# Kernel optimization log

Hardware: AMD Instinct MI355X
Metric: run time of the kernel (lower is better)

The kernel has to match this reference:

```python
import jax, jax.numpy as jnp
import numpy as np

N = 50000        # nodes
E = 800000       # edges (before self loops)
G = 512          # graphs
H = 2            # heads
FIN = 128        # in_features
CH = 64          # hidden per head
COUT = 32        # out_features
NEG_SLOPE = 0.2  # PyG GATConv default
BN_EPS = 1e-5


def _gat(x, src, dst, W, a_src, a_dst, b, concat, n):
    # x: [n, F], W: [F, H*C], a_src/a_dst: [H, C]
    h = (x @ W).reshape(n, a_src.shape[0], a_src.shape[1])        # [n, H, C]
    e = jax.nn.leaky_relu((h * a_src).sum(-1)[src]
                          + (h * a_dst).sum(-1)[dst], NEG_SLOPE)  # [Etot, H]
    # per-destination segment softmax (self loops guarantee nonempty segments)
    m = jax.ops.segment_max(e, dst, num_segments=n)
    ex = jnp.exp(e - m[dst])
    s = jax.ops.segment_sum(ex, dst, num_segments=n)
    alpha = ex / (s[dst] + 1e-16)                                 # [Etot, H]
    out = jax.ops.segment_sum(h[src] * alpha[:, :, None], dst, num_segments=n)
    out = out.reshape(n, -1) if concat else out.mean(axis=1)
    return out + b


def _bn(x, gamma, beta, mean, var):
    # BatchNorm1d in eval mode (running statistics)
    return (x - mean) * jax.lax.rsqrt(var + BN_EPS) * gamma + beta


def setup_inputs() -> dict:
    key = jax.random.key(0)
    ks = jax.random.split(key, 12)
    x = jax.random.normal(ks[0], (N, FIN), dtype=jnp.float32)
    edge_index = jax.random.randint(ks[1], (2, E), 0, N, dtype=jnp.int32)
    batch = jnp.sort(jax.random.randint(ks[2], (N,), 0, G, dtype=jnp.int32))
    inp = {"x": x, "edge_index": edge_index, "batch": batch}
    # layer 1: GATConv(FIN -> CH, heads=H, concat=True)
    inp["W1"] = jax.random.normal(ks[3], (FIN, H * CH), dtype=jnp.float32) * 0.1
    inp["as1"] = jax.random.normal(ks[4], (H, CH), dtype=jnp.float32) * 0.1
    inp["ad1"] = jax.random.normal(ks[5], (H, CH), dtype=jnp.float32) * 0.1
    inp["b1"] = jnp.zeros((H * CH,), dtype=jnp.float32)
    inp["bn1_gamma"] = jnp.ones((H * CH,), dtype=jnp.float32)
    inp["bn1_beta"] = jnp.zeros((H * CH,), dtype=jnp.float32)
    inp["bn1_mean"] = jax.random.normal(ks[6], (H * CH,), dtype=jnp.float32) * 0.05
    inp["bn1_var"] = jnp.ones((H * CH,), dtype=jnp.float32)
    # layer 2: GATConv(H*CH -> COUT, heads=H, concat=False)
    inp["W2"] = jax.random.normal(ks[7], (H * CH, H * COUT), dtype=jnp.float32) * 0.1
    inp["as2"] = jax.random.normal(ks[8], (H, COUT), dtype=jnp.float32) * 0.1
    inp["ad2"] = jax.random.normal(ks[9], (H, COUT), dtype=jnp.float32) * 0.1
    inp["b2"] = jnp.zeros((COUT,), dtype=jnp.float32)
    inp["bn2_gamma"] = jnp.ones((COUT,), dtype=jnp.float32)
    inp["bn2_beta"] = jnp.zeros((COUT,), dtype=jnp.float32)
    inp["bn2_mean"] = jax.random.normal(ks[10], (COUT,), dtype=jnp.float32) * 0.05
    inp["bn2_var"] = jnp.ones((COUT,), dtype=jnp.float32)
    return inp


def reference(x, edge_index, batch,
              W1, as1, ad1, b1, bn1_gamma, bn1_beta, bn1_mean, bn1_var,
              W2, as2, ad2, b2, bn2_gamma, bn2_beta, bn2_mean, bn2_var):
    n = x.shape[0]
    sl = jnp.arange(n, dtype=edge_index.dtype)
    src = jnp.concatenate([edge_index[0], sl])  # PyG add_self_loops=True
    dst = jnp.concatenate([edge_index[1], sl])
    h = _gat(x, src, dst, W1, as1, ad1, b1, True, n)
    h = jax.nn.relu(_bn(h, bn1_gamma, bn1_beta, bn1_mean, bn1_var))
    h = _gat(h, src, dst, W2, as2, ad2, b2, False, n)
    h = _bn(h, bn2_gamma, bn2_beta, bn2_mean, bn2_var)
    # global mean pool over graphs
    sums = jax.ops.segment_sum(h, batch, num_segments=G)
    cnts = jax.ops.segment_sum(jnp.ones((n,), h.dtype), batch, num_segments=G)
    pooled = sums / jnp.maximum(cnts, 1.0)[:, None]
    return jax.nn.log_softmax(pooled, axis=1)
```

## Files before the change

### kernel.cpp

```cpp
#include <hip/hip_runtime.h>
#include <hip/hip_bf16.h>

#define NEG_SLOPE 0.2f
#define BN_EPS 1e-5f
#define BSHIFT 7
#define P_PART 256
#define MAXB 512

typedef unsigned int uint32;
typedef unsigned short ushort16;
typedef __attribute__((ext_vector_type(8))) short bf16x8;
typedef __attribute__((ext_vector_type(4))) float f32x4;
typedef __attribute__((ext_vector_type(2))) float f32x2;

__device__ __forceinline__ ushort16 f2bf(float f) {
    uint32 u = __float_as_uint(f);
    u = (u + 0x7fff + ((u >> 16) & 1)) >> 16;
    return (ushort16)u;
}

__device__ __forceinline__ f32x2 pkfma(f32x2 ex2, uint32 u, f32x2 acc) {
    f32x2 f;
    f.x = __uint_as_float(u << 16);
    f.y = __uint_as_float(u & 0xffff0000u);
    asm("v_pk_fma_f32 %0, %1, %2, %0" : "+v"(acc) : "v"(ex2), "v"(f));
    return acc;
}

__device__ __forceinline__ void scan_bbase(const int* __restrict__ rowtot, int nbuck,
                                           int Etot, int* sb ) {
    const int t = threadIdx.x;
    int v0 = (t < nbuck) ? rowtot[t] : 0;
    int v1 = (256 + t < nbuck) ? rowtot[256 + t] : 0;
    sb[t] = v0;
    sb[256 + t] = v1;
    __syncthreads();
    for (int off = 1; off < 512; off <<= 1) {
        int a0 = (t >= off) ? sb[t - off] : 0;
        int a1 = (256 + t >= off) ? sb[256 + t - off] : 0;
        __syncthreads();
        sb[t] += a0;
        sb[256 + t] += a1;
        __syncthreads();
    }
    int i0 = sb[t], i1 = sb[256 + t];
    __syncthreads();
    sb[t] = i0 - v0;
    sb[256 + t] = i1 - v1;
    if (t == 0) sb[MAXB] = Etot;
    __syncthreads();
}

template <int OC, int C>
__device__ __forceinline__ void pack_col(int col, int k, const float* __restrict__ W,
                                         const float* __restrict__ a_s,
                                         const float* __restrict__ a_d,
                                         ushort16* __restrict__ wt) {
    float v = 0.f;
    if (col < OC) {
        v = W[k * OC + col];
    } else if (col < OC + 2) {
        int hh = col - OC;
        float s = 0.f;
        for (int c = 0; c < C; ++c) s += W[k * OC + hh * C + c] * a_s[hh * C + c];
        v = s;
    } else if (col < OC + 4) {
        int hh = col - OC - 2;
        float s = 0.f;
        for (int c = 0; c < C; ++c) s += W[k * OC + hh * C + c] * a_d[hh * C + c];
        v = s;
    }
    wt[(size_t)col * 128 + k] = f2bf(v);
}

template <int OC, int NT, bool AF32>
__device__ __forceinline__ void gemm_body(int gb, const void* __restrict__ xin,
                                          const ushort16* __restrict__ wt,
                                          ushort16* __restrict__ h, float4* __restrict__ att,
                                          float2* __restrict__ asc, int N) {
    const int wave = threadIdx.x >> 6, lane = threadIdx.x & 63;
    const int tile = gb * 4 + wave;
    if (tile * 16 >= N) return;
    const int m = lane & 15, quad = lane >> 4;
    const int node = tile * 16 + m;

    bf16x8 a[4];
    if (AF32) {
        const float* xr = (const float*)xin + (size_t)node * 128 + quad * 8;
#pragma unroll
        for (int c = 0; c < 4; ++c) {
            float4 u = *(const float4*)(xr + c * 32);
            float4 v = *(const float4*)(xr + c * 32 + 4);
            bf16x8 t;
            t[0] = (short)f2bf(u.x); t[1] = (short)f2bf(u.y);
            t[2] = (short)f2bf(u.z); t[3] = (short)f2bf(u.w);
            t[4] = (short)f2bf(v.x); t[5] = (short)f2bf(v.y);
            t[6] = (short)f2bf(v.z); t[7] = (short)f2bf(v.w);
            a[c] = t;
        }
    } else {
        const ushort16* xr = (const ushort16*)xin + (size_t)node * 128 + quad * 8;
#pragma unroll
        for (int c = 0; c < 4; ++c) a[c] = *(const bf16x8*)(xr + c * 32);
    }

    for (int t = 0; t < NT; ++t) {
        const ushort16* wr = wt + ((size_t)(t * 16 + m)) * 128 + quad * 8;
        bf16x8 b[4];
#pragma unroll
        for (int c = 0; c < 4; ++c) b[c] = *(const bf16x8*)(wr + c * 32);
        f32x4 acc = {0.f, 0.f, 0.f, 0.f};
#pragma unroll
        for (int c = 0; c < 4; ++c)
            acc = __builtin_amdgcn_mfma_f32_16x16x32_bf16(a[c], b[c], acc, 0, 0, 0);
        if (t * 16 < OC) {
#pragma unroll
            for (int r = 0; r < 4; ++r) {
                int nrow = tile * 16 + quad * 4 + r;
                h[(size_t)nrow * OC + t * 16 + m] = f2bf(acc[r]);
            }
        } else if (m < 4) {
#pragma unroll
            for (int r = 0; r < 4; ++r) {
                int nrow = tile * 16 + quad * 4 + r;
                ((float*)(att + nrow))[m] = acc[r];
                if (m < 2) ((float*)(asc + nrow))[m] = acc[r];
            }
        }
    }
}

__global__ __launch_bounds__(256) void fused_prep(
    const int* __restrict__ ei, int E, int Etot, int nbuck, int chunk, int* __restrict__ hist,
    const float* __restrict__ W1, const float* __restrict__ as1, const float* __restrict__ ad1,
    ushort16* __restrict__ wt1,
    const float* __restrict__ W2, const float* __restrict__ as2, const float* __restrict__ ad2,
    ushort16* __restrict__ wt2,
    const float* __restrict__ b1, const float* __restrict__ g1, const float* __restrict__ be1,
    const float* __restrict__ mu1, const float* __restrict__ vr1,
    const float* __restrict__ b2, const float* __restrict__ g2, const float* __restrict__ be2,
    const float* __restrict__ mu2, const float* __restrict__ vr2,
    float2* __restrict__ bn1, float2* __restrict__ bn2,
    const int* __restrict__ batch, int N, int G, int* __restrict__ gstart) {
    const int bid = blockIdx.x;
    if (bid < P_PART) {
        __shared__ int lh[MAXB];
        const int p = bid;
        for (int i = threadIdx.x; i < nbuck; i += 256) lh[i] = 0;
        __syncthreads();
        const int beg = p * chunk;
        const int end = min(beg + chunk, Etot);
        for (int i = beg + threadIdx.x; i < end; i += 256) {
            int d = (i < E) ? ei[E + i] : i - E;
            atomicAdd(&lh[d >> BSHIFT], 1);
        }
        __syncthreads();
        for (int i = threadIdx.x; i < nbuck; i += 256) hist[(size_t)i * P_PART + p] = lh[i];
        return;
    }
    int rb = bid - P_PART;
    if (rb < 72) {
        pack_col<128, 64>(rb * 2 + (threadIdx.x >> 7), threadIdx.x & 127, W1, as1, ad1, wt1);
        return;
    }
    rb -= 72;
    if (rb < 40) {
        pack_col<64, 32>(rb * 2 + (threadIdx.x >> 7), threadIdx.x & 127, W2, as2, ad2, wt2);
        return;
    }
    rb -= 40;
    if (rb == 0) {
        const int c = threadIdx.x;
        if (c < 128) {
            float A = g1[c] * rsqrtf(vr1[c] + BN_EPS);
            bn1[c] = make_float2(A, A * (b1[c] - mu1[c]) + be1[c]);
        } else if (c < 160) {
            const int c2 = c - 128;
            float A = g2[c2] * rsqrtf(vr2[c2] + BN_EPS);
            bn2[c2] = make_float2(A, A * (b2[c2] - mu2[c2]) + be2[c2]);
        }
        return;
    }
    rb -= 1;
    {
        int g = rb * 256 + (int)threadIdx.x;
        if (g > G) return;
        if (g == G) { gstart[G] = N; return; }
        int lo = 0, hi = N;
        while (lo < hi) { int mid = (lo + hi) >> 1; if (batch[mid] < g) lo = mid + 1; else hi = mid; }
        gstart[g] = lo;
    }
}

__global__ __launch_bounds__(P_PART) void row_scan(int* __restrict__ hist,
                                                   int* __restrict__ rowtot) {
    const int b = blockIdx.x;
    __shared__ int s[P_PART];
    const int t = threadIdx.x;
    int v = hist[(size_t)b * P_PART + t];
    s[t] = v;
    __syncthreads();
    for (int off = 1; off < P_PART; off <<= 1) {
        int u = (t >= off) ? s[t - off] : 0;
        __syncthreads();
        s[t] += u;
        __syncthreads();
    }
    hist[(size_t)b * P_PART + t] = s[t] - v;
    if (t == P_PART - 1) rowtot[b] = s[t];
}

__global__ __launch_bounds__(256) void fused_scatter_gemm1(
    const int* __restrict__ ei, int E, int Etot, int nbuck, int chunk,
    const int* __restrict__ hist, const int* __restrict__ rowtot, uint32* __restrict__ ebuf,
    const void* __restrict__ x, const ushort16* __restrict__ wt1,
    ushort16* __restrict__ h1, float4* __restrict__ att1, float2* __restrict__ asc1, int N) {
    const int bid = blockIdx.x;
    if (bid < P_PART) {
        __shared__ int sb[MAXB + 1];
        __shared__ int cur[MAXB];
        scan_bbase(rowtot, nbuck, Etot, sb);
        const int p = bid;
        for (int i = threadIdx.x; i < nbuck; i += 256)
            cur[i] = sb[i] + hist[(size_t)i * P_PART + p];
        __syncthreads();
        const int beg = p * chunk;
        const int end = min(beg + chunk, Etot);
        for (int i = beg + threadIdx.x; i < end; i += 256) {
            int s_, d_;
            if (i < E) { s_ = ei[i]; d_ = ei[E + i]; }
            else       { s_ = d_ = i - E; }
            int pos = atomicAdd(&cur[d_ >> BSHIFT], 1);
            ebuf[pos] = ((uint32)(d_ & ((1 << BSHIFT) - 1)) << 25) | (uint32)s_;
        }
    } else {
        gemm_body<128, 9, true>(bid - P_PART, x, wt1, h1, att1, asc1, N);
    }
}

__global__ __launch_bounds__(256) void bucket_place(
    const int* __restrict__ rowtot, int nbuck, int Etot, const uint32* __restrict__ ebuf,
    int N, int* __restrict__ base, int* __restrict__ csr_src) {
    const int bk = blockIdx.x;
    __shared__ int sb[MAXB + 1];
    __shared__ int ldeg[1 << BSHIFT];
    __shared__ int sscan[1 << BSHIFT];
    __shared__ int lcur[1 << BSHIFT];
    scan_bbase(rowtot, nbuck, Etot, sb);
    const int t = threadIdx.x;
    if (t < (1 << BSHIFT)) { ldeg[t] = 0; lcur[t] = 0; }
    __syncthreads();
    const int beg = sb[bk], end = sb[bk + 1];
    for (int i = beg + t; i < end; i += 256) atomicAdd(&ldeg[ebuf[i] >> 25], 1);
    __syncthreads();
    if (t < 128) sscan[t] = ldeg[t];
    __syncthreads();
    for (int off = 1; off < 128; off <<= 1) {
        int v = 0;
        if (t < 128 && t >= off) v = sscan[t - off];
        __syncthreads();
        if (t < 128) sscan[t] += v;
        __syncthreads();
    }
    if (t < 128) {
        int node = (bk << BSHIFT) + t;
        if (node < N) base[node] = beg + sscan[t] - ldeg[t];
    }
    __syncthreads();
    for (int i = beg + t; i < end; i += 256) {
        uint32 pk = ebuf[i];
        int dl = (int)(pk >> 25);
        int s_ = (int)(pk & 0x1FFFFFFu);
        int pos = beg + (sscan[dl] - ldeg[dl]) + atomicAdd(&lcur[dl], 1);
        csr_src[pos] = s_;
    }
}

__global__ __launch_bounds__(256) void gemm2_kernel(
    const void* __restrict__ xin, const ushort16* __restrict__ wt,
    ushort16* __restrict__ h, float4* __restrict__ att, float2* __restrict__ asc, int N) {
    gemm_body<64, 5, false>(blockIdx.x, xin, wt, h, att, asc, N);
}

__global__ __launch_bounds__(256) void gat_gather1(
    const int* __restrict__ base, const int* __restrict__ csr_src, int Etot, int N,
    const ushort16* __restrict__ h, const float4* __restrict__ att,
    const float2* __restrict__ asc, const float2* __restrict__ bn1,
    ushort16* __restrict__ outb) {
    const int tid = threadIdx.x;
    const int node = blockIdx.x * 16 + (tid >> 4);
    if (node >= N) return;
    const int t = tid & 63;
    const int q = tid & 15;
    const int gbase = t & 48;
    const int hh = q >> 3;
    const int hbit = q & 8;
    const int eh = q & 7;
    const int beg = base[node];
    const int end = (node + 1 < N) ? base[node + 1] : Etot;
    const int deg = end - beg;
    const float4 adn = att[node];
    const float ad = hh ? adn.w : adn.z;
    const char* hq = (const char*)h + q * 16;

    f32x2 ac0 = {0.f, 0.f}, ac1 = {0.f, 0.f}, ac2 = {0.f, 0.f}, ac3 = {0.f, 0.f};
    float ssum = 0.f;

    int sidxme = csr_src[beg + ((eh < deg) ? eh : 0)];

    for (int c0e = 0; c0e < deg; c0e += 8) {
        const int degc = min(deg - c0e, 8);
        const bool ok = eh < degc;
        const int offme = sidxme << 8;
        const float av = ((const float*)asc)[2 * sidxme + hh];
        uint4 hv[8];
#pragma unroll
        for (int s = 0; s < 8; ++s) {
            const int ofs = __shfl(offme, gbase + s, 64);
            hv[s] = *(const uint4*)(hq + ofs);
        }
        const int nb = c0e + 8;
        const int na = (nb < deg) ? (nb + ((eh < deg - nb) ? eh : 0)) : 0;
        const int sidx_next = csr_src[beg + na];
        float e = av + ad;
        e = e > 0.f ? e : NEG_SLOPE * e;
        const float x = ok ? __expf(e) : 0.f;
        float r = x;
#pragma unroll
        for (int off = 1; off < 8; off <<= 1) r += __shfl_xor(r, off, 64);
        ssum += r;
#pragma unroll
        for (int e0 = 0; e0 < 8; e0 += 4) {
            if (e0 < degc) {
#pragma unroll
                for (int j = 0; j < 4; ++j) {
                    const float ex = __shfl(x, (gbase + e0 + j) | hbit, 64);
                    f32x2 ex2; ex2.x = ex; ex2.y = ex;
                    ac0 = pkfma(ex2, hv[e0 + j].x, ac0);
                    ac1 = pkfma(ex2, hv[e0 + j].y, ac1);
                    ac2 = pkfma(ex2, hv[e0 + j].z, ac2);
                    ac3 = pkfma(ex2, hv[e0 + j].w, ac3);
                }
            }
        }
        sidxme = sidx_next;
    }
    const float inv = 1.f / (ssum + 1e-16f);
    const int c0 = 8 * q;
    const float4* bp = (const float4*)(bn1 + c0);
    const float4 w0 = bp[0], w1 = bp[1], w2 = bp[2], w3 = bp[3];
    float va[8] = {ac0.x, ac0.y, ac1.x, ac1.y, ac2.x, ac2.y, ac3.x, ac3.y};
    float Ac[8] = {w0.x, w0.z, w1.x, w1.z, w2.x, w2.z, w3.x, w3.z};
    float Cc[8] = {w0.y, w0.w, w1.y, w1.w, w2.y, w2.w, w3.y, w3.w};
    uint32 pk[4];
#pragma unroll
    for (int i = 0; i < 8; i += 2) {
        float v0 = fmaxf(fmaf(Ac[i], va[i] * inv, Cc[i]), 0.f);
        float v1 = fmaxf(fmaf(Ac[i + 1], va[i + 1] * inv, Cc[i + 1]), 0.f);
        pk[i >> 1] = (uint32)f2bf(v0) | ((uint32)f2bf(v1) << 16);
    }
    *(uint4*)(outb + (size_t)node * 128 + c0) = make_uint4(pk[0], pk[1], pk[2], pk[3]);
}

__global__ __launch_bounds__(256) void gat_gather2(
    const int* __restrict__ base, const int* __restrict__ csr_src, int Etot, int N,
    const ushort16* __restrict__ h2, const float4* __restrict__ att,
    const float2* __restrict__ asc, const float2* __restrict__ bn2,
    float* __restrict__ node_out) {
    const int tid = threadIdx.x;
    const int node = blockIdx.x * 16 + (tid >> 4);
    if (node >= N) return;
    const int t = tid & 63;
    const int q = tid & 15;
    const int gbase = t & 48;
    const int hh = q >> 3;
    const int hbit = q & 8;
    const int eh = q & 7;
    const int beg = base[node];
    const int end = (node + 1 < N) ? base[node + 1] : Etot;
    const int deg = end - beg;
    const float4 adn = att[node];
    const float ad = hh ? adn.w : adn.z;
    const char* hq = (const char*)h2 + q * 8;

    f32x2 ac0 = {0.f, 0.f}, ac1 = {0.f, 0.f};
    float ssum = 0.f;

    int sidxme = csr_src[beg + ((eh < deg) ? eh : 0)];

    for (int c0e = 0; c0e < deg; c0e += 8) {
        const int degc = min(deg - c0e, 8);
        const bool ok = eh < degc;
        const int offme = sidxme << 7;
        const float av = ((const float*)asc)[2 * sidxme + hh];
        uint2 hv[8];
#pragma unroll
        for (int s = 0; s < 8; ++s) {
            const int ofs = __shfl(offme, gbase + s, 64);
            hv[s] = *(const uint2*)(hq + ofs);
        }
        const int nb = c0e + 8;
        const int na = (nb < deg) ? (nb + ((eh < deg - nb) ? eh : 0)) : 0;
        const int sidx_next = csr_src[beg + na];
        float e = av + ad;
        e = e > 0.f ? e : NEG_SLOPE * e;
        const float x = ok ? __expf(e) : 0.f;
        float r = x;
#pragma unroll
        for (int off = 1; off < 8; off <<= 1) r += __shfl_xor(r, off, 64);
        ssum += r;
#pragma unroll
        for (int e0 = 0; e0 < 8; e0 += 4) {
            if (e0 < degc) {
#pragma unroll
                for (int j = 0; j < 4; ++j) {
                    const float ex = __shfl(x, (gbase + e0 + j) | hbit, 64);
                    f32x2 ex2; ex2.x = ex; ex2.y = ex;
                    ac0 = pkfma(ex2, hv[e0 + j].x, ac0);
                    ac1 = pkfma(ex2, hv[e0 + j].y, ac1);
                }
            }
        }
        sidxme = sidx_next;
    }
    const float inv = 1.f / (ssum + 1e-16f);
    float v0 = ac0.x * inv, v1 = ac0.y * inv, v2 = ac1.x * inv, v3 = ac1.y * inv;
    const int psrc = gbase | ((q + 8) & 15);
    float p0 = __shfl(v0, psrc, 64);
    float p1 = __shfl(v1, psrc, 64);
    float p2 = __shfl(v2, psrc, 64);
    float p3 = __shfl(v3, psrc, 64);
    if (q < 8) {
        const int c0 = 4 * q;
        const float4* bp = (const float4*)(bn2 + c0);
        const float4 w0 = bp[0], w1 = bp[1];
        float m0 = fmaf(w0.x, 0.5f * (v0 + p0), w0.y);
        float m1 = fmaf(w0.z, 0.5f * (v1 + p1), w0.w);
        float m2 = fmaf(w1.x, 0.5f * (v2 + p2), w1.y);
        float m3 = fmaf(w1.z, 0.5f * (v3 + p3), w1.w);
        *(float4*)(node_out + (size_t)node * 32 + c0) = make_float4(m0, m1, m2, m3);
    }
}

__global__ __launch_bounds__(256) void pool_logsoftmax(
    const float* __restrict__ node_out, const int* __restrict__ gstart,
    float* __restrict__ out) {
    const int gidx = blockIdx.x;
    const int tid = threadIdx.x;
    const int c = tid & 31, r = tid >> 5;
    const int n0 = gstart[gidx], n1 = gstart[gidx + 1];
    float s = 0.f;
    for (int n = n0 + r; n < n1; n += 8) s += node_out[(size_t)n * 32 + c];
    __shared__ float red[8][32];
    red[r][c] = s;
    __syncthreads();
    if (r == 0) {
        float tot = red[0][c];
#pragma unroll
        for (int k = 1; k < 8; ++k) tot += red[k][c];
        float v = tot / fmaxf((float)(n1 - n0), 1.f);
        float m = v;
#pragma unroll
        for (int off = 16; off >= 1; off >>= 1) m = fmaxf(m, __shfl_xor(m, off, 64));
        float ex = __expf(v - m);
        float ssum = ex;
#pragma unroll
        for (int off = 16; off >= 1; off >>= 1) ssum += __shfl_xor(ssum, off, 64);
        out[gidx * 32 + c] = v - m - logf(ssum);
    }
}

extern "C" void kernel_launch(void* const* d_in, const int* in_sizes, int n_in,
                              void* d_out, int out_size, void* d_ws, size_t ws_size,
                              hipStream_t stream) {
    const float* x   = (const float*)d_in[0];
    const int* ei    = (const int*)d_in[1];
    const int* batch = (const int*)d_in[2];
    const float* W1  = (const float*)d_in[3];
    const float* as1 = (const float*)d_in[4];
    const float* ad1 = (const float*)d_in[5];
    const float* b1  = (const float*)d_in[6];
    const float* g1  = (const float*)d_in[7];
    const float* be1 = (const float*)d_in[8];
    const float* mu1 = (const float*)d_in[9];
    const float* vr1 = (const float*)d_in[10];
    const float* W2  = (const float*)d_in[11];
    const float* as2 = (const float*)d_in[12];
    const float* ad2 = (const float*)d_in[13];
    const float* b2  = (const float*)d_in[14];
    const float* g2  = (const float*)d_in[15];
    const float* be2 = (const float*)d_in[16];
    const float* mu2 = (const float*)d_in[17];
    const float* vr2 = (const float*)d_in[18];
    float* out = (float*)d_out;

    const int N = in_sizes[0] / 128;
    const int E = in_sizes[1] / 2;
    const int Etot = E + N;
    const int G = out_size / 32;
    const int nbuck = (N + (1 << BSHIFT) - 1) >> BSHIFT;
    const int chunk = (Etot + P_PART - 1) / P_PART;
    const int M = nbuck * P_PART;
    const int ntile = (N + 15) / 16;
    const int gemm_grid = (ntile + 3) / 4;
    const int gbb = (G + 1 + 255) / 256;

    float* p = (float*)d_ws;
    size_t o = 0;
    auto al = [&]() { o = (o + 3) & ~(size_t)3; };
    ushort16* h1b   = (ushort16*)(p + o); o += (size_t)N * 64;  al();
    ushort16* agg1b = (ushort16*)(p + o); o += (size_t)N * 64;  al();
    ushort16* h2b   = (ushort16*)(p + o); o += (size_t)N * 32;  al();
    float4* att1 = (float4*)(p + o); o += (size_t)N * 4;  al();
    float4* att2 = (float4*)(p + o); o += (size_t)N * 4;  al();
    float2* asc1 = (float2*)(p + o); o += (size_t)N * 2;  al();
    float2* asc2 = (float2*)(p + o); o += (size_t)N * 2;  al();
    float* nodeo = p + o; o += (size_t)N * 32; al();
    ushort16* wt1 = (ushort16*)(p + o); o += (size_t)144 * 64; al();
    ushort16* wt2 = (ushort16*)(p + o); o += (size_t)80 * 64;  al();
    float2* bn1  = (float2*)(p + o); o += (size_t)128 * 2; al();
    float2* bn2  = (float2*)(p + o); o += (size_t)32 * 2;  al();
    int* csr_src = (int*)(p + o); o += (size_t)Etot; al();
    uint32* ebuf = (uint32*)(p + o); o += (size_t)Etot; al();
    int* base    = (int*)(p + o); o += (size_t)N;    al();
    int* hist    = (int*)(p + o); o += (size_t)M;    al();
    int* rowtot  = (int*)(p + o); o += (size_t)nbuck + 4; al();
    int* gstart  = (int*)(p + o); o += (size_t)G + 4; al();

    fused_prep<<<P_PART + 72 + 40 + 1 + gbb, 256, 0, stream>>>(
        ei, E, Etot, nbuck, chunk, hist, W1, as1, ad1, wt1, W2, as2, ad2, wt2,
        b1, g1, be1, mu1, vr1, b2, g2, be2, mu2, vr2, bn1, bn2,
        batch, N, G, gstart);
    row_scan<<<nbuck, P_PART, 0, stream>>>(hist, rowtot);
    fused_scatter_gemm1<<<P_PART + gemm_grid, 256, 0, stream>>>(
        ei, E, Etot, nbuck, chunk, hist, rowtot, ebuf, x, wt1, h1b, att1, asc1, N);
    bucket_place<<<nbuck, 256, 0, stream>>>(rowtot, nbuck, Etot, ebuf, N, base, csr_src);
    gat_gather1<<<(N + 15) / 16, 256, 0, stream>>>(base, csr_src, Etot, N, h1b, att1, asc1,
                                                   bn1, agg1b);
    gemm2_kernel<<<gemm_grid, 256, 0, stream>>>(agg1b, wt2, h2b, att2, asc2, N);
    gat_gather2<<<(N + 15) / 16, 256, 0, stream>>>(base, csr_src, Etot, N, h2b, att2, asc2,
                                                   bn2, nodeo);
    pool_logsoftmax<<<G, 256, 0, stream>>>(nodeo, gstart, out);
}
```

Baseline: 211.9 us.

## Fuse layer-2 GEMM into gather1 and pool via atomics in gather2

The layer-2 projection GEMM now runs inside gat_gather1. Each block stages its 16 aggregated bf16 rows in LDS and runs MFMA against wt2, so the agg1b intermediate and a separate kernel launch disappear. gat_gather2 now atomically adds per-node outputs into per-graph sums, zeroed in fused_prep, and a small finish kernel applies the mean and log-softmax. This removes two global round-trips and two launches, at the cost of a __syncthreads in gather1, idle waves during the small GEMM, and contention on float atomics, which also make the summation order nondeterministic.

```diff
diff --git a/kernel.cpp b/kernel.cpp
--- a/kernel.cpp
+++ b/kernel.cpp
@@ -140,7 +140,7 @@
     const float* __restrict__ mu1, const float* __restrict__ vr1,
     const float* __restrict__ b2, const float* __restrict__ g2, const float* __restrict__ be2,
     const float* __restrict__ mu2, const float* __restrict__ vr2,
-    float2* __restrict__ bn1, float2* __restrict__ bn2,
+    float2* __restrict__ bn1, float2* __restrict__ bn2, float* __restrict__ graphsum,
     const int* __restrict__ batch, int N, int G, int* __restrict__ gstart) {
     const int bid = blockIdx.x;
     if (bid < P_PART) {
@@ -182,6 +182,13 @@
         return;
     }
     rb -= 1;
+    const int zb = (G * 32 + 255) >> 8;
+    if (rb < zb) {
+        int idx = rb * 256 + (int)threadIdx.x;
+        if (idx < G * 32) graphsum[idx] = 0.f;
+        return;
+    }
+    rb -= zb;
     {
         int g = rb * 256 + (int)threadIdx.x;
         if (g > G) return;
@@ -276,17 +283,137 @@
     }
 }
 
-__global__ __launch_bounds__(256) void gemm2_kernel(
-    const void* __restrict__ xin, const ushort16* __restrict__ wt,
-    ushort16* __restrict__ h, float4* __restrict__ att, float2* __restrict__ asc, int N) {
-    gemm_body<64, 5, false>(blockIdx.x, xin, wt, h, att, asc, N);
-}
-
 __global__ __launch_bounds__(256) void gat_gather1(
     const int* __restrict__ base, const int* __restrict__ csr_src, int Etot, int N,
     const ushort16* __restrict__ h, const float4* __restrict__ att,
     const float2* __restrict__ asc, const float2* __restrict__ bn1,
-    ushort16* __restrict__ outb) {
+    const ushort16* __restrict__ wt2, ushort16* __restrict__ h2,
+    float4* __restrict__ att2, float2* __restrict__ asc2) {
+    __shared__ char agg_lds[16 * 272];
+    const int tid = threadIdx.x;
+    const int nr = tid >> 4;
+    const int node = blockIdx.x * 16 + nr;
+    const bool live = node < N;
+    const int t = tid & 63;
+    const int q = tid & 15;
+    const int gbase = t & 48;
+    const int hh = q >> 3;
+    const int hbit = q & 8;
+    const int eh = q & 7;
+    int beg = 0, deg = 0;
+    float ad = 0.f;
+    if (live) {
+        beg = base[node];
+        const int end = (node + 1 < N) ? base[node + 1] : Etot;
+        deg = end - beg;
+        const float4 adn = att[node];
+        ad = hh ? adn.w : adn.z;
+    }
+    const char* hq = (const char*)h + q * 16;
+
+    f32x2 ac0 = {0.f, 0.f}, ac1 = {0.f, 0.f}, ac2 = {0.f, 0.f}, ac3 = {0.f, 0.f};
+    float ssum = 0.f;
+
+    int sidxme = csr_src[beg + ((eh < deg) ? eh : 0)];
+
+    for (int c0e = 0; c0e < deg; c0e += 8) {
+        const int degc = min(deg - c0e, 8);
+        const bool ok = eh < degc;
+        const int offme = sidxme << 8;
+        const float av = ((const float*)asc)[2 * sidxme + hh];
+        uint4 hv[8];
+#pragma unroll
+        for (int s = 0; s < 8; ++s) {
+            const int ofs = __shfl(offme, gbase + s, 64);
+            hv[s] = *(const uint4*)(hq + ofs);
+        }
+        const int nb = c0e + 8;
+        const int na = (nb < deg) ? (nb + ((eh < deg - nb) ? eh : 0)) : 0;
+        const int sidx_next = csr_src[beg + na];
+        float e = av + ad;
+        e = e > 0.f ? e : NEG_SLOPE * e;
+        const float x = ok ? __expf(e) : 0.f;
+        float r = x;
+#pragma unroll
+        for (int off = 1; off < 8; off <<= 1) r += __shfl_xor(r, off, 64);
+        ssum += r;
+#pragma unroll
+        for (int e0 = 0; e0 < 8; e0 += 4) {
+            if (e0 < degc) {
+#pragma unroll
+                for (int j = 0; j < 4; ++j) {
+                    const float ex = __shfl(x, (gbase + e0 + j) | hbit, 64);
+                    f32x2 ex2; ex2.x = ex; ex2.y = ex;
+                    ac0 = pkfma(ex2, hv[e0 + j].x, ac0);
+                    ac1 = pkfma(ex2, hv[e0 + j].y, ac1);
+                    ac2 = pkfma(ex2, hv[e0 + j].z, ac2);
+                    ac3 = pkfma(ex2, hv[e0 + j].w, ac3);
+                }
+            }
+        }
+        sidxme = sidx_next;
+    }
+    const float inv = 1.f / (ssum + 1e-16f);
+    const int c0 = 8 * q;
+    const float4* bp = (const float4*)(bn1 + c0);
+    const float4 w0 = bp[0], w1 = bp[1], w2 = bp[2], w3 = bp[3];
+    float va[8] = {ac0.x, ac0.y, ac1.x, ac1.y, ac2.x, ac2.y, ac3.x, ac3.y};
+    float Ac[8] = {w0.x, w0.z, w1.x, w1.z, w2.x, w2.z, w3.x, w3.z};
+    float Cc[8] = {w0.y, w0.w, w1.y, w1.w, w2.y, w2.w, w3.y, w3.w};
+    uint32 pk[4];
+#pragma unroll
+    for (int i = 0; i < 8; i += 2) {
+        float v0 = fmaxf(fmaf(Ac[i], va[i] * inv, Cc[i]), 0.f);
+        float v1 = fmaxf(fmaf(Ac[i + 1], va[i + 1] * inv, Cc[i + 1]), 0.f);
+        pk[i >> 1] = (uint32)f2bf(v0) | ((uint32)f2bf(v1) << 16);
+    }
+    *(uint4*)(agg_lds + nr * 272 + q * 16) = make_uint4(pk[0], pk[1], pk[2], pk[3]);
+    __syncthreads();
+
+    const int wave = tid >> 6;
+    const int m = t & 15, quad = t >> 4;
+    bf16x8 a[4];
+#pragma unroll
+    for (int c = 0; c < 4; ++c)
+        a[c] = *(const bf16x8*)(agg_lds + m * 272 + quad * 16 + c * 64);
+    const int tile0 = blockIdx.x * 16;
+#pragma unroll
+    for (int tt = 0; tt < 2; ++tt) {
+        const int tcol = wave + tt * 4;
+        if (tcol < 5) {
+            const ushort16* wr = wt2 + ((size_t)(tcol * 16 + m)) * 128 + quad * 8;
+            bf16x8 b[4];
+#pragma unroll
+            for (int c = 0; c < 4; ++c) b[c] = *(const bf16x8*)(wr + c * 32);
+            f32x4 acc = {0.f, 0.f, 0.f, 0.f};
+#pragma unroll
+            for (int c = 0; c < 4; ++c)
+                acc = __builtin_amdgcn_mfma_f32_16x16x32_bf16(a[c], b[c], acc, 0, 0, 0);
+            if (tcol * 16 < 64) {
+#pragma unroll
+                for (int r = 0; r < 4; ++r) {
+                    int nrow = tile0 + quad * 4 + r;
+                    if (nrow < N) h2[(size_t)nrow * 64 + tcol * 16 + m] = f2bf(acc[r]);
+                }
+            } else if (m < 4) {
+#pragma unroll
+                for (int r = 0; r < 4; ++r) {
+                    int nrow = tile0 + quad * 4 + r;
+                    if (nrow < N) {
+                        ((float*)(att2 + nrow))[m] = acc[r];
+                        if (m < 2) ((float*)(asc2 + nrow))[m] = acc[r];
+                    }
+                }
+            }
+        }
+    }
+}
+
+__global__ __launch_bounds__(256) void gat_gather2(
+    const int* __restrict__ base, const int* __restrict__ csr_src, int Etot, int N,
+    const ushort16* __restrict__ h2, const float4* __restrict__ att,
+    const float2* __restrict__ asc, const float2* __restrict__ bn2,
+    const int* __restrict__ batch, float* __restrict__ graphsum) {
     const int tid = threadIdx.x;
     const int node = blockIdx.x * 16 + (tid >> 4);
     if (node >= N) return;
@@ -296,86 +423,7 @@
     const int hh = q >> 3;
     const int hbit = q & 8;
     const int eh = q & 7;
-    const int beg = base[node];
-    const int end = (node + 1 < N) ? base[node + 1] : Etot;
-    const int deg = end - beg;
-    const float4 adn = att[node];
-    const float ad = hh ? adn.w : adn.z;
-    const char* hq = (const char*)h + q * 16;
-
-    f32x2 ac0 = {0.f, 0.f}, ac1 = {0.f, 0.f}, ac2 = {0.f, 0.f}, ac3 = {0.f, 0.f};
-    float ssum = 0.f;
-
-    int sidxme = csr_src[beg + ((eh < deg) ? eh : 0)];
-
-    for (int c0e = 0; c0e < deg; c0e += 8) {
-        const int degc = min(deg - c0e, 8);
-        const bool ok = eh < degc;
-        const int offme = sidxme << 8;
-        const float av = ((const float*)asc)[2 * sidxme + hh];
-        uint4 hv[8];
-#pragma unroll
-        for (int s = 0; s < 8; ++s) {
-            const int ofs = __shfl(offme, gbase + s, 64);
-            hv[s] = *(const uint4*)(hq + ofs);
-        }
-        const int nb = c0e + 8;
-        const int na = (nb < deg) ? (nb + ((eh < deg - nb) ? eh : 0)) : 0;
-        const int sidx_next = csr_src[beg + na];
-        float e = av + ad;
-        e = e > 0.f ? e : NEG_SLOPE * e;
-        const float x = ok ? __expf(e) : 0.f;
-        float r = x;
-#pragma unroll
-        for (int off = 1; off < 8; off <<= 1) r += __shfl_xor(r, off, 64);
-        ssum += r;
-#pragma unroll
-        for (int e0 = 0; e0 < 8; e0 += 4) {
-            if (e0 < degc) {
-#pragma unroll
-                for (int j = 0; j < 4; ++j) {
-                    const float ex = __shfl(x, (gbase + e0 + j) | hbit, 64);
-                    f32x2 ex2; ex2.x = ex; ex2.y = ex;
-                    ac0 = pkfma(ex2, hv[e0 + j].x, ac0);
-                    ac1 = pkfma(ex2, hv[e0 + j].y, ac1);
-                    ac2 = pkfma(ex2, hv[e0 + j].z, ac2);
-                    ac3 = pkfma(ex2, hv[e0 + j].w, ac3);
-                }
-            }
-        }
-        sidxme = sidx_next;
-    }
-    const float inv = 1.f / (ssum + 1e-16f);
-    const int c0 = 8 * q;
-    const float4* bp = (const float4*)(bn1 + c0);
-    const float4 w0 = bp[0], w1 = bp[1], w2 = bp[2], w3 = bp[3];
-    float va[8] = {ac0.x, ac0.y, ac1.x, ac1.y, ac2.x, ac2.y, ac3.x, ac3.y};
-    float Ac[8] = {w0.x, w0.z, w1.x, w1.z, w2.x, w2.z, w3.x, w3.z};
-    float Cc[8] = {w0.y, w0.w, w1.y, w1.w, w2.y, w2.w, w3.y, w3.w};
-    uint32 pk[4];
-#pragma unroll
-    for (int i = 0; i < 8; i += 2) {
-        float v0 = fmaxf(fmaf(Ac[i], va[i] * inv, Cc[i]), 0.f);
-        float v1 = fmaxf(fmaf(Ac[i + 1], va[i + 1] * inv, Cc[i + 1]), 0.f);
-        pk[i >> 1] = (uint32)f2bf(v0) | ((uint32)f2bf(v1) << 16);
-    }
-    *(uint4*)(outb + (size_t)node * 128 + c0) = make_uint4(pk[0], pk[1], pk[2], pk[3]);
-}
-
-__global__ __launch_bounds__(256) void gat_gather2(
-    const int* __restrict__ base, const int* __restrict__ csr_src, int Etot, int N,
-    const ushort16* __restrict__ h2, const float4* __restrict__ att,
-    const float2* __restrict__ asc, const float2* __restrict__ bn2,
-    float* __restrict__ node_out) {
-    const int tid = threadIdx.x;
-    const int node = blockIdx.x * 16 + (tid >> 4);
-    if (node >= N) return;
-    const int t = tid & 63;
-    const int q = tid & 15;
-    const int gbase = t & 48;
-    const int hh = q >> 3;
-    const int hbit = q & 8;
-    const int eh = q & 7;
+    const int gid = batch[node];
     const int beg = base[node];
     const int end = (node + 1 < N) ? base[node + 1] : Etot;
     const int deg = end - beg;
@@ -438,36 +486,30 @@
         float m1 = fmaf(w0.z, 0.5f * (v1 + p1), w0.w);
         float m2 = fmaf(w1.x, 0.5f * (v2 + p2), w1.y);
         float m3 = fmaf(w1.z, 0.5f * (v3 + p3), w1.w);
-        *(float4*)(node_out + (size_t)node * 32 + c0) = make_float4(m0, m1, m2, m3);
-    }
-}
-
-__global__ __launch_bounds__(256) void pool_logsoftmax(
-    const float* __restrict__ node_out, const int* __restrict__ gstart,
+        float* gs = graphsum + (size_t)gid * 32 + c0;
+        atomicAdd(gs + 0, m0);
+        atomicAdd(gs + 1, m1);
+        atomicAdd(gs + 2, m2);
+        atomicAdd(gs + 3, m3);
+    }
+}
+
+__global__ __launch_bounds__(64) void pool_finish(
+    const float* __restrict__ graphsum, const int* __restrict__ gstart,
     float* __restrict__ out) {
-    const int gidx = blockIdx.x;
-    const int tid = threadIdx.x;
-    const int c = tid & 31, r = tid >> 5;
-    const int n0 = gstart[gidx], n1 = gstart[gidx + 1];
-    float s = 0.f;
-    for (int n = n0 + r; n < n1; n += 8) s += node_out[(size_t)n * 32 + c];
-    __shared__ float red[8][32];
-    red[r][c] = s;
-    __syncthreads();
-    if (r == 0) {
-        float tot = red[0][c];
-#pragma unroll
-        for (int k = 1; k < 8; ++k) tot += red[k][c];
-        float v = tot / fmaxf((float)(n1 - n0), 1.f);
-        float m = v;
-#pragma unroll
-        for (int off = 16; off >= 1; off >>= 1) m = fmaxf(m, __shfl_xor(m, off, 64));
-        float ex = __expf(v - m);
-        float ssum = ex;
-#pragma unroll
-        for (int off = 16; off >= 1; off >>= 1) ssum += __shfl_xor(ssum, off, 64);
-        out[gidx * 32 + c] = v - m - logf(ssum);
-    }
+    const int g = blockIdx.x;
+    if (threadIdx.x >= 32) return;
+    const int c = threadIdx.x;
+    const int n0 = gstart[g], n1 = gstart[g + 1];
+    float v = graphsum[(size_t)g * 32 + c] / fmaxf((float)(n1 - n0), 1.f);
+    float m = v;
+#pragma unroll
+    for (int off = 16; off >= 1; off >>= 1) m = fmaxf(m, __shfl_xor(m, off, 32));
+    float ex = __expf(v - m);
+    float s = ex;
+#pragma unroll
+    for (int off = 16; off >= 1; off >>= 1) s += __shfl_xor(s, off, 32);
+    out[g * 32 + c] = v - m - logf(s);
 }
 
 extern "C" void kernel_launch(void* const* d_in, const int* in_sizes, int n_in,
@@ -504,22 +546,22 @@
     const int ntile = (N + 15) / 16;
     const int gemm_grid = (ntile + 3) / 4;
     const int gbb = (G + 1 + 255) / 256;
+    const int zb = (G * 32 + 255) / 256;
 
     float* p = (float*)d_ws;
     size_t o = 0;
     auto al = [&]() { o = (o + 3) & ~(size_t)3; };
     ushort16* h1b   = (ushort16*)(p + o); o += (size_t)N * 64;  al();
-    ushort16* agg1b = (ushort16*)(p + o); o += (size_t)N * 64;  al();
     ushort16* h2b   = (ushort16*)(p + o); o += (size_t)N * 32;  al();
     float4* att1 = (float4*)(p + o); o += (size_t)N * 4;  al();
     float4* att2 = (float4*)(p + o); o += (size_t)N * 4;  al();
     float2* asc1 = (float2*)(p + o); o += (size_t)N * 2;  al();
     float2* asc2 = (float2*)(p + o); o += (size_t)N * 2;  al();
-    float* nodeo = p + o; o += (size_t)N * 32; al();
     ushort16* wt1 = (ushort16*)(p + o); o += (size_t)144 * 64; al();
     ushort16* wt2 = (ushort16*)(p + o); o += (size_t)80 * 64;  al();
     float2* bn1  = (float2*)(p + o); o += (size_t)128 * 2; al();
     float2* bn2  = (float2*)(p + o); o += (size_t)32 * 2;  al();
+    float* graphsum = p + o; o += (size_t)G * 32; al();
     int* csr_src = (int*)(p + o); o += (size_t)Etot; al();
     uint32* ebuf = (uint32*)(p + o); o += (size_t)Etot; al();
     int* base    = (int*)(p + o); o += (size_t)N;    al();
@@ -527,18 +569,17 @@
     int* rowtot  = (int*)(p + o); o += (size_t)nbuck + 4; al();
     int* gstart  = (int*)(p + o); o += (size_t)G + 4; al();
 
-    fused_prep<<<P_PART + 72 + 40 + 1 + gbb, 256, 0, stream>>>(
+    fused_prep<<<P_PART + 72 + 40 + 1 + zb + gbb, 256, 0, stream>>>(
         ei, E, Etot, nbuck, chunk, hist, W1, as1, ad1, wt1, W2, as2, ad2, wt2,
-        b1, g1, be1, mu1, vr1, b2, g2, be2, mu2, vr2, bn1, bn2,
+        b1, g1, be1, mu1, vr1, b2, g2, be2, mu2, vr2, bn1, bn2, graphsum,
         batch, N, G, gstart);
     row_scan<<<nbuck, P_PART, 0, stream>>>(hist, rowtot);
     fused_scatter_gemm1<<<P_PART + gemm_grid, 256, 0, stream>>>(
         ei, E, Etot, nbuck, chunk, hist, rowtot, ebuf, x, wt1, h1b, att1, asc1, N);
     bucket_place<<<nbuck, 256, 0, stream>>>(rowtot, nbuck, Etot, ebuf, N, base, csr_src);
-    gat_gather1<<<(N + 15) / 16, 256, 0, stream>>>(base, csr_src, Etot, N, h1b, att1, asc1,
-                                                   bn1, agg1b);
-    gemm2_kernel<<<gemm_grid, 256, 0, stream>>>(agg1b, wt2, h2b, att2, asc2, N);
-    gat_gather2<<<(N + 15) / 16, 256, 0, stream>>>(base, csr_src, Etot, N, h2b, att2, asc2,
-                                                   bn2, nodeo);
-    pool_logsoftmax<<<G, 256, 0, stream>>>(nodeo, gstart, out);
-}
+    gat_gather1<<<ntile, 256, 0, stream>>>(base, csr_src, Etot, N, h1b, att1, asc1,
+                                           bn1, wt2, h2b, att2, asc2);
+    gat_gather2<<<ntile, 256, 0, stream>>>(base, csr_src, Etot, N, h2b, att2, asc2,
+                                           bn2, batch, graphsum);
+    pool_finish<<<G, 64, 0, stream>>>(graphsum, gstart, out);
+}
```

Result: slower. 243.3 us (+14.8%).
